# Performance work log

Hardware: AMD Instinct MI355X
Metric: run time of the kernel (lower is better)

## Reference

```python
import jax, jax.numpy as jnp
import numpy as np

B, S, D = 4, 2048, 1024
H = 16
DK = D // H  # 64
THETA = 10000.0


def setup_inputs() -> dict:
    key = jax.random.key(0)
    ks = jax.random.split(key, 5)
    scale = 1.0 / np.sqrt(D)
    return {
        "x": jax.random.normal(ks[0], (B, S, D), dtype=jnp.float32),
        "wq": jax.random.normal(ks[1], (D, D), dtype=jnp.float32) * scale,
        "wk": jax.random.normal(ks[2], (D, D), dtype=jnp.float32) * scale,
        "wv": jax.random.normal(ks[3], (D, D), dtype=jnp.float32) * scale,
        "wo": jax.random.normal(ks[4], (D, D), dtype=jnp.float32) * scale,
    }


def _rope(x, cos2, sin2):
    # x: [B, H, S, DK]; cos2/sin2: [S, DK]
    x_even = x[..., 0::2]
    x_odd = x[..., 1::2]
    x_rot = jnp.stack([-x_odd, x_even], axis=-1).reshape(x.shape)
    return x * cos2 + x_rot * sin2


def reference(x, wq, wk, wv, wo):
    b, s, d = x.shape
    # QKV projections (weights are [out, in]; y = x @ W^T)
    q = jnp.einsum("bsd,od->bso", x, wq).reshape(b, s, H, DK).swapaxes(1, 2)
    k = jnp.einsum("bsd,od->bso", x, wk).reshape(b, s, H, DK).swapaxes(1, 2)
    v = jnp.einsum("bsd,od->bso", x, wv).reshape(b, s, H, DK).swapaxes(1, 2)

    # RoPE tables for positions [0, s)
    inv_freq = 1.0 / (THETA ** (jnp.arange(0, DK, 2, dtype=jnp.float32) / DK))
    angles = jnp.arange(s, dtype=jnp.float32)[:, None] * inv_freq[None, :]  # [s, DK/2]
    cos2 = jnp.repeat(jnp.cos(angles), 2, axis=-1).astype(x.dtype)  # [s, DK]
    sin2 = jnp.repeat(jnp.sin(angles), 2, axis=-1).astype(x.dtype)
    q = _rope(q, cos2, sin2)
    k = _rope(k, cos2, sin2)

    # Naive quadratic attention with causal mask (matches source sdpa)
    scores = jnp.einsum("bhqd,bhkd->bhqk", q, k) / (DK ** 0.5)
    causal = jnp.tril(jnp.ones((s, s), dtype=jnp.float32))
    scores = jnp.where(causal == 0.0, -jnp.inf, scores)
    probs = jax.nn.softmax(scores, axis=-1)
    attn = jnp.einsum("bhqk,bhkd->bhqd", probs, v)

    attn = attn.swapaxes(1, 2).reshape(b, s, d)
    return jnp.einsum("bsd,od->bso", attn, wo)
```

## Files before the change

### kernel.cpp

```cpp
#include <hip/hip_runtime.h>


typedef _Float16 f16;
typedef _Float16 f16x4 __attribute__((ext_vector_type(4)));
typedef _Float16 f16x8 __attribute__((ext_vector_type(8)));
typedef float    f32x4 __attribute__((ext_vector_type(4)));
typedef __fp16   h16x2 __attribute__((ext_vector_type(2)));

typedef __attribute__((address_space(1))) void gvoid_t;
typedef __attribute__((address_space(3))) void lvoid_t;

#define GLD16(g, l) __builtin_amdgcn_global_load_lds( \
    (gvoid_t*)(const void*)(g), (lvoid_t*)(l), 16, 0, 0)

#define VMCNT(n) asm volatile("s_waitcnt vmcnt(" #n ")" ::: "memory")

__device__ __forceinline__ void bar() {
    __builtin_amdgcn_sched_barrier(0);
    __builtin_amdgcn_s_barrier();
    __builtin_amdgcn_sched_barrier(0);
}

constexpr int BB = 4, SS = 2048, DD = 1024, HH = 16, DKK = 64;
constexpr int MM = BB * SS;

__global__ void cvt_kernel(const float4* __restrict__ in, f16x4* __restrict__ out, int n4) {
    int stride = gridDim.x * blockDim.x;
    for (int i = blockIdx.x * blockDim.x + threadIdx.x; i < n4; i += stride) {
        float4 v = in[i];
        f16x4 o;
        o[0] = (f16)v.x; o[1] = (f16)v.y; o[2] = (f16)v.z; o[3] = (f16)v.w;
        out[i] = o;
    }
}

__global__ void cvt4_kernel(const float4* __restrict__ a, const float4* __restrict__ b,
                            const float4* __restrict__ c, const float4* __restrict__ d,
                            f16x4* __restrict__ out, int n4per) {
    const float4* srcs[4] = {a, b, c, d};
    const float4* src = srcs[blockIdx.y];
    f16x4* dst = out + (size_t)blockIdx.y * n4per;
    int stride = gridDim.x * blockDim.x;
    for (int i = blockIdx.x * blockDim.x + threadIdx.x; i < n4per; i += stride) {
        float4 v = src[i];
        f16x4 o;
        o[0] = (f16)v.x; o[1] = (f16)v.y; o[2] = (f16)v.z; o[3] = (f16)v.w;
        dst[i] = o;
    }
}

__global__ void rope_tab_kernel(float* __restrict__ ctab, float* __restrict__ stab) {
    int idx = blockIdx.x * blockDim.x + threadIdx.x;
    if (idx >= SS * DKK) return;
    int s = idx >> 6, dk = idx & 63, i = dk >> 1;
    float inv = powf(10000.0f, -(float)(2 * i) / (float)DKK);
    float ang = (float)s * inv;
    ctab[idx] = cosf(ang);
    stab[idx] = sinf(ang);
}

__device__ __forceinline__ void gemm_core(
    const f16* __restrict__ A, const f16* __restrict__ Bm,
    f16* As, f16* Bs, f32x4 (&acc)[4][4], int bm, int bn)
{
    const int tid  = threadIdx.x;
    const int lane = tid & 63, wid = tid >> 6;
    const int lrow = lane & 15, lk = lane >> 4;
    const int wm = (wid >> 1) * 64, wn = (wid & 1) * 64;

    const int r_ = tid >> 3, c_ = tid & 7;

    auto STAGE = [&](int buf, int k0) {
#pragma unroll
        for (int j = 0; j < 4; ++j) {
            int r = j * 32 + r_;
            int cs = (c_ ^ (r & 7)) * 8;
            GLD16(A  + (size_t)(bm + r) * 1024 + k0 + cs, As + buf * 8192 + (j * 256 + wid * 64) * 8);
            GLD16(Bm + (size_t)(bn + r) * 1024 + k0 + cs, Bs + buf * 8192 + (j * 256 + wid * 64) * 8);
        }
    };

    auto COMPUTE = [&](int buf) {
        const f16* Ab = As + buf * 8192;
        const f16* Bb = Bs + buf * 8192;
#pragma unroll
        for (int kk = 0; kk < 2; ++kk) {
            f16x8 af[4], bf[4];
#pragma unroll
            for (int mi = 0; mi < 4; ++mi) {
                int row = wm + mi * 16 + lrow;
                af[mi] = *(const f16x8*)&Ab[row * 64 + ((kk * 4 + lk) ^ (row & 7)) * 8];
            }
#pragma unroll
            for (int ni = 0; ni < 4; ++ni) {
                int row = wn + ni * 16 + lrow;
                bf[ni] = *(const f16x8*)&Bb[row * 64 + ((kk * 4 + lk) ^ (row & 7)) * 8];
            }
#pragma unroll
            for (int mi = 0; mi < 4; ++mi)
#pragma unroll
                for (int ni = 0; ni < 4; ++ni)
                    acc[mi][ni] = __builtin_amdgcn_mfma_f32_16x16x32_f16(
                        af[mi], bf[ni], acc[mi][ni], 0, 0, 0);
        }
    };

    STAGE(0, 0);
    int cur = 0;
#pragma unroll 1
    for (int t = 0; t < 16; ++t) {
        if (t < 15) { STAGE(cur ^ 1, (t + 1) * 64); VMCNT(8); }
        else        { VMCNT(0); }
        bar();
        COMPUTE(cur);
        bar();
        cur ^= 1;
    }
}

__global__ __launch_bounds__(256) void qkv_gemm(
    const f16* __restrict__ xb, const f16* __restrict__ wqkv,
    f16* __restrict__ Qr, f16* __restrict__ Kr, f16* __restrict__ Vt,
    const float* __restrict__ ctab, const float* __restrict__ stab)
{
    __shared__ __align__(16) f16 As[2 * 128 * 64];
    __shared__ __align__(16) f16 Bs[2 * 128 * 64];
    const int i = blockIdx.x;
    const int xcol = i >> 6;
    const int yrow = (i & 7) * 8 + ((i >> 3) & 7);
    const int bm = yrow * 128, bn = xcol * 128;
    const int z = bn >> 10;
    const int bnw = bn & 1023;

    f32x4 acc[4][4] = {};
    gemm_core(xb, wqkv, As, Bs, acc, bm, bn);

    const int tid = threadIdx.x, lane = tid & 63, wid = tid >> 6;
    const int lrow = lane & 15, lk = lane >> 4;
    const int wm = (wid >> 1) * 64, wn = (wid & 1) * 64;

    if (z == 2) {
#pragma unroll
        for (int mi = 0; mi < 4; ++mi)
#pragma unroll
            for (int ni = 0; ni < 4; ++ni)
#pragma unroll
                for (int r = 0; r < 4; ++r) {
                    int row = bm + wm + mi * 16 + lk * 4 + r;
                    int col = bnw + wn + ni * 16 + lrow;
                    int b = row >> 11, s = row & 2047, h = col >> 6, dk = col & 63;
                    Vt[((size_t)(b * HH + h) * DKK + dk) * SS + s] = (f16)acc[mi][ni][r];
                }
    } else {
        f16* Out = (z == 0) ? Qr : Kr;
        const float scale = (z == 0) ? 0.125f * 1.44269504088896f : 1.0f;
#pragma unroll
        for (int mi = 0; mi < 4; ++mi)
#pragma unroll
            for (int ni = 0; ni < 4; ++ni)
#pragma unroll
                for (int r = 0; r < 4; ++r) {
                    int row = bm + wm + mi * 16 + lk * 4 + r;
                    int col = bnw + wn + ni * 16 + lrow;
                    int b = row >> 11, s = row & 2047, h = col >> 6, dk = col & 63;
                    float v = acc[mi][ni][r];
                    float partner = __shfl_xor(v, 1);
                    float cc = ctab[s * DKK + dk], ssn = stab[s * DKK + dk];
                    float rot = (col & 1) ? partner : -partner;
                    float o = (v * cc + rot * ssn) * scale;
                    Out[((size_t)(b * HH + h) * SS + s) * DKK + dk] = (f16)o;
                }
    }
}

__global__ __launch_bounds__(256, 4) void attn_kernel(
    const f16* __restrict__ Q, const f16* __restrict__ K, const f16* __restrict__ Vt,
    f16* __restrict__ attnB)
{
    __shared__ __align__(16) f16 Ks[2][64 * 64];
    __shared__ __align__(16) f16 Vs[2][64 * 64];
    __shared__ __align__(16) f16 Ps[4][16 * 64];

    const int tid = threadIdx.x, lane = tid & 63, wid = tid >> 6;
    const int lrow = lane & 15, lk = lane >> 4;
    const int bx = blockIdx.x;
    const int qt = 15 - (bx >> 6);
    const int bh = (bx & 7) * 8 + ((bx >> 3) & 7);
    const int b = bh >> 4, h = bh & 15;

    const f16* Qb = Q  + (size_t)bh * SS * DKK;
    const f16* Kb = K  + (size_t)bh * SS * DKK;
    const f16* Vb = Vt + (size_t)bh * DKK * SS;
    f16* PsW = &Ps[wid][0];

    const int qw = qt * 128 + wid * 32;
    const int nt = 2 * qt + 2;

    f16x8 qf[2][2];
#pragma unroll
    for (int mi = 0; mi < 2; ++mi)
#pragma unroll
        for (int kk = 0; kk < 2; ++kk)
            qf[mi][kk] = *(const f16x8*)&Qb[(size_t)(qw + mi * 16 + lrow) * DKK + kk * 32 + lk * 8];

    f32x4 oacc[2][4] = {};
    float mst[2] = {-1e30f, -1e30f}, lst[2] = {0.0f, 0.0f};
    int cur = 0;

#pragma unroll
    for (int j = 0; j < 2; ++j) {
        int ci = j * 256 + tid;
        int r = ci >> 3, c = ci & 7;
        int cs = (c ^ (r & 7)) * 8;
        GLD16(Kb + (size_t)r * DKK + cs, &Ks[cur][(j * 256 + wid * 64) * 8]);
        GLD16(Vb + (size_t)r * SS  + cs, &Vs[cur][(j * 256 + wid * 64) * 8]);
    }

#pragma unroll 1
    for (int t = 0; t < nt; ++t) {
        const int kv0 = t * 64;
        if (t + 1 < nt) {
            const int kvn = kv0 + 64;
#pragma unroll
            for (int j = 0; j < 2; ++j) {
                int ci = j * 256 + tid;
                int r = ci >> 3, c = ci & 7;
                int cs = (c ^ (r & 7)) * 8;
                GLD16(Kb + (size_t)(kvn + r) * DKK + cs, &Ks[cur ^ 1][(j * 256 + wid * 64) * 8]);
                GLD16(Vb + (size_t)r * SS + kvn + cs,    &Vs[cur ^ 1][(j * 256 + wid * 64) * 8]);
            }
            VMCNT(4);
        } else {
            VMCNT(0);
        }
        bar();

        if (kv0 <= qw + 31) {
            f32x4 sacc[2][4] = {};
            __builtin_amdgcn_s_setprio(1);
#pragma unroll
            for (int kk = 0; kk < 2; ++kk)
#pragma unroll
                for (int ni = 0; ni < 4; ++ni) {
                    int row = ni * 16 + lrow;
                    f16x8 kf = *(const f16x8*)&Ks[cur][row * 64 + ((kk * 4 + lk) ^ (row & 7)) * 8];
#pragma unroll
                    for (int mi = 0; mi < 2; ++mi)
                        sacc[mi][ni] = __builtin_amdgcn_mfma_f32_16x16x32_f16(
                            kf, qf[mi][kk], sacc[mi][ni], 0, 0, 0);
                }
            __builtin_amdgcn_s_setprio(0);

#pragma unroll
            for (int mi = 0; mi < 2; ++mi) {
                const int q = qw + mi * 16 + lrow;
                if (kv0 + 63 > q) {
#pragma unroll
                    for (int ni = 0; ni < 4; ++ni)
#pragma unroll
                        for (int r = 0; r < 4; ++r)
                            if (kv0 + ni * 16 + lk * 4 + r > q) sacc[mi][ni][r] = -1e30f;
                }
                float m0 = -1e30f;
#pragma unroll
                for (int ni = 0; ni < 4; ++ni) {
                    float a = fmaxf(sacc[mi][ni][0], sacc[mi][ni][1]);
                    float bx2 = fmaxf(sacc[mi][ni][2], sacc[mi][ni][3]);
                    m0 = fmaxf(m0, fmaxf(a, bx2));
                }
                m0 = fmaxf(m0, __shfl_xor(m0, 16));
                m0 = fmaxf(m0, __shfl_xor(m0, 32));
                if (!__all(m0 - mst[mi] <= 11.5f)) {
                    const float mnew  = fmaxf(mst[mi], m0);
                    const float alpha = exp2f(mst[mi] - mnew);
                    mst[mi] = mnew;
                    lst[mi] *= alpha;
#pragma unroll
                    for (int no = 0; no < 4; ++no)
#pragma unroll
                        for (int r = 0; r < 4; ++r)
                            oacc[mi][no][r] *= alpha;
                }
                const float mref = mst[mi];
                float rsum = 0.0f;
#pragma unroll
                for (int ni = 0; ni < 4; ++ni) {
                    float p0 = exp2f(sacc[mi][ni][0] - mref);
                    float p1 = exp2f(sacc[mi][ni][1] - mref);
                    float p2 = exp2f(sacc[mi][ni][2] - mref);
                    float p3 = exp2f(sacc[mi][ni][3] - mref);
                    rsum += (p0 + p1) + (p2 + p3);
                    h16x2 w0 = __builtin_amdgcn_cvt_pkrtz(p0, p1);
                    h16x2 w1 = __builtin_amdgcn_cvt_pkrtz(p2, p3);
                    f16x4 w;
                    w[0] = (f16)w0[0]; w[1] = (f16)w0[1];
                    w[2] = (f16)w1[0]; w[3] = (f16)w1[1];
                    const int c = ni * 2 + (lk >> 1);
                    *(f16x4*)&PsW[lrow * 64 + ((c ^ (lrow & 7)) * 8) + (lk & 1) * 4] = w;
                }
                rsum += __shfl_xor(rsum, 16);
                rsum += __shfl_xor(rsum, 32);
                lst[mi] += rsum;

                f16x8 pa[2];
#pragma unroll
                for (int kk = 0; kk < 2; ++kk)
                    pa[kk] = *(const f16x8*)&PsW[lrow * 64 + ((kk * 4 + lk) ^ (lrow & 7)) * 8];
                __builtin_amdgcn_s_setprio(1);
#pragma unroll
                for (int kk = 0; kk < 2; ++kk)
#pragma unroll
                    for (int no = 0; no < 4; ++no) {
                        int row = no * 16 + lrow;
                        f16x8 vf = *(const f16x8*)&Vs[cur][row * 64 + ((kk * 4 + lk) ^ (row & 7)) * 8];
                        oacc[mi][no] = __builtin_amdgcn_mfma_f32_16x16x32_f16(
                            vf, pa[kk], oacc[mi][no], 0, 0, 0);
                    }
                __builtin_amdgcn_s_setprio(0);
            }
        }

        bar();
        cur ^= 1;
    }

#pragma unroll
    for (int mi = 0; mi < 2; ++mi) {
        const float rl = 1.0f / lst[mi];
        const int q = qw + mi * 16 + lrow;
#pragma unroll
        for (int no = 0; no < 4; ++no) {
            f16x4 w;
#pragma unroll
            for (int r = 0; r < 4; ++r) w[r] = (f16)(oacc[mi][no][r] * rl);
            *(f16x4*)&attnB[((size_t)(b * SS) + q) * DD + h * DKK + no * 16 + lk * 4] = w;
        }
    }
}

__global__ __launch_bounds__(256) void out_gemm(
    const f16* __restrict__ attnB, const f16* __restrict__ wob, float* __restrict__ out)
{
    __shared__ __align__(16) f16 As[2 * 128 * 64];
    __shared__ __align__(16) f16 Bs[2 * 128 * 64];
    const int i = blockIdx.x;
    const int xcol = i >> 6;
    const int yrow = (i & 7) * 8 + ((i >> 3) & 7);
    const int bm = yrow * 128, bn = xcol * 128;
    f32x4 acc[4][4] = {};
    gemm_core(attnB, wob, As, Bs, acc, bm, bn);
    const int tid = threadIdx.x, lane = tid & 63, wid = tid >> 6;
    const int lrow = lane & 15, lk = lane >> 4;
    const int wm = (wid >> 1) * 64, wn = (wid & 1) * 64;
#pragma unroll
    for (int mi = 0; mi < 4; ++mi)
#pragma unroll
        for (int ni = 0; ni < 4; ++ni)
#pragma unroll
            for (int r = 0; r < 4; ++r) {
                int row = bm + wm + mi * 16 + lk * 4 + r;
                int col = bn + wn + ni * 16 + lrow;
                out[(size_t)row * 1024 + col] = acc[mi][ni][r];
            }
}

extern "C" void kernel_launch(void* const* d_in, const int* in_sizes, int n_in,
                              void* d_out, int out_size, void* d_ws, size_t ws_size,
                              hipStream_t stream) {
    const float* x  = (const float*)d_in[0];
    const float* wq = (const float*)d_in[1];
    const float* wk = (const float*)d_in[2];
    const float* wv = (const float*)d_in[3];
    const float* wo = (const float*)d_in[4];
    float* out = (float*)d_out;

    constexpr size_t NXB = (size_t)MM * DD;
    constexpr size_t NW  = (size_t)DD * DD;
    f16* xb  = (f16*)d_ws;
    f16* wqkv = xb + NXB;
    f16* wob  = wqkv + 3 * NW;
    f16* Qr  = wob + NW;
    f16* Kr  = Qr  + NXB;
    f16* Vt  = Kr  + NXB;
    float* ctab = (float*)(Vt + NXB);
    float* stab = ctab + SS * DKK;
    f16* attnB = xb;

    cvt_kernel<<<2048, 256, 0, stream>>>((const float4*)x, (f16x4*)xb, (int)(NXB / 4));
    cvt4_kernel<<<dim3(512, 4), 256, 0, stream>>>((const float4*)wq, (const float4*)wk,
                                                  (const float4*)wv, (const float4*)wo,
                                                  (f16x4*)wqkv, (int)(NW / 4));
    rope_tab_kernel<<<(SS * DKK + 255) / 256, 256, 0, stream>>>(ctab, stab);

    qkv_gemm<<<1536, 256, 0, stream>>>(xb, wqkv, Qr, Kr, Vt, ctab, stab);
    attn_kernel<<<1024, 256, 0, stream>>>(Qr, Kr, Vt, attnB);
    out_gemm<<<512, 256, 0, stream>>>(attnB, wob, out);
}
```

Measured before the change: 207.3 us.

## Shrink attention query tile to 64 rows, one 16-row slab per wave

The attention kernel now gives each block 64 query rows instead of 128, with each wave handling 16 rows instead of 32, and launches twice as many blocks. The causal-skip branch and the setprio hints are removed, since every wave's tile now intersects every loaded KV tile. This doubles parallelism and cuts the wasted causal work per block. In exchange, K/V tiles are reused by half as many query rows, so K/V global traffic doubles and each LDS K/V read feeds fewer MFMAs.

Result: faster. 179.0 us (-13.7%).

```diff
diff --git a/kernel.cpp b/kernel.cpp
--- a/kernel.cpp
+++ b/kernel.cpp
@@ -184,7 +184,7 @@
     const int tid = threadIdx.x, lane = tid & 63, wid = tid >> 6;
     const int lrow = lane & 15, lk = lane >> 4;
     const int bx = blockIdx.x;
-    const int qt = 15 - (bx >> 6);
+    const int qt = 31 - (bx >> 6);
     const int bh = (bx & 7) * 8 + ((bx >> 3) & 7);
     const int b = bh >> 4, h = bh & 15;
 
@@ -193,18 +193,17 @@
     const f16* Vb = Vt + (size_t)bh * DKK * SS;
     f16* PsW = &Ps[wid][0];
 
-    const int qw = qt * 128 + wid * 32;
-    const int nt = 2 * qt + 2;
-
-    f16x8 qf[2][2];
-#pragma unroll
-    for (int mi = 0; mi < 2; ++mi)
-#pragma unroll
-        for (int kk = 0; kk < 2; ++kk)
-            qf[mi][kk] = *(const f16x8*)&Qb[(size_t)(qw + mi * 16 + lrow) * DKK + kk * 32 + lk * 8];
-
-    f32x4 oacc[2][4] = {};
-    float mst[2] = {-1e30f, -1e30f}, lst[2] = {0.0f, 0.0f};
+    const int qw = qt * 64 + wid * 16;
+    const int nt = qt + 1;
+    const int q  = qw + lrow;
+
+    f16x8 qf[2];
+#pragma unroll
+    for (int kk = 0; kk < 2; ++kk)
+        qf[kk] = *(const f16x8*)&Qb[(size_t)q * DKK + kk * 32 + lk * 8];
+
+    f32x4 oacc[4] = {};
+    float mst = -1e30f, lst = 0.0f;
     int cur = 0;
 
 #pragma unroll
@@ -235,104 +234,90 @@
         }
         bar();
 
-        if (kv0 <= qw + 31) {
-            f32x4 sacc[2][4] = {};
-            __builtin_amdgcn_s_setprio(1);
-#pragma unroll
-            for (int kk = 0; kk < 2; ++kk)
-#pragma unroll
-                for (int ni = 0; ni < 4; ++ni) {
-                    int row = ni * 16 + lrow;
-                    f16x8 kf = *(const f16x8*)&Ks[cur][row * 64 + ((kk * 4 + lk) ^ (row & 7)) * 8];
-#pragma unroll
-                    for (int mi = 0; mi < 2; ++mi)
-                        sacc[mi][ni] = __builtin_amdgcn_mfma_f32_16x16x32_f16(
-                            kf, qf[mi][kk], sacc[mi][ni], 0, 0, 0);
-                }
-            __builtin_amdgcn_s_setprio(0);
-
-#pragma unroll
-            for (int mi = 0; mi < 2; ++mi) {
-                const int q = qw + mi * 16 + lrow;
-                if (kv0 + 63 > q) {
-#pragma unroll
-                    for (int ni = 0; ni < 4; ++ni)
-#pragma unroll
-                        for (int r = 0; r < 4; ++r)
-                            if (kv0 + ni * 16 + lk * 4 + r > q) sacc[mi][ni][r] = -1e30f;
-                }
-                float m0 = -1e30f;
-#pragma unroll
-                for (int ni = 0; ni < 4; ++ni) {
-                    float a = fmaxf(sacc[mi][ni][0], sacc[mi][ni][1]);
-                    float bx2 = fmaxf(sacc[mi][ni][2], sacc[mi][ni][3]);
-                    m0 = fmaxf(m0, fmaxf(a, bx2));
-                }
-                m0 = fmaxf(m0, __shfl_xor(m0, 16));
-                m0 = fmaxf(m0, __shfl_xor(m0, 32));
-                if (!__all(m0 - mst[mi] <= 11.5f)) {
-                    const float mnew  = fmaxf(mst[mi], m0);
-                    const float alpha = exp2f(mst[mi] - mnew);
-                    mst[mi] = mnew;
-                    lst[mi] *= alpha;
-#pragma unroll
-                    for (int no = 0; no < 4; ++no)
-#pragma unroll
-                        for (int r = 0; r < 4; ++r)
-                            oacc[mi][no][r] *= alpha;
-                }
-                const float mref = mst[mi];
-                float rsum = 0.0f;
-#pragma unroll
-                for (int ni = 0; ni < 4; ++ni) {
-                    float p0 = exp2f(sacc[mi][ni][0] - mref);
-                    float p1 = exp2f(sacc[mi][ni][1] - mref);
-                    float p2 = exp2f(sacc[mi][ni][2] - mref);
-                    float p3 = exp2f(sacc[mi][ni][3] - mref);
-                    rsum += (p0 + p1) + (p2 + p3);
-                    h16x2 w0 = __builtin_amdgcn_cvt_pkrtz(p0, p1);
-                    h16x2 w1 = __builtin_amdgcn_cvt_pkrtz(p2, p3);
-                    f16x4 w;
-                    w[0] = (f16)w0[0]; w[1] = (f16)w0[1];
-                    w[2] = (f16)w1[0]; w[3] = (f16)w1[1];
-                    const int c = ni * 2 + (lk >> 1);
-                    *(f16x4*)&PsW[lrow * 64 + ((c ^ (lrow & 7)) * 8) + (lk & 1) * 4] = w;
-                }
-                rsum += __shfl_xor(rsum, 16);
-                rsum += __shfl_xor(rsum, 32);
-                lst[mi] += rsum;
-
-                f16x8 pa[2];
-#pragma unroll
-                for (int kk = 0; kk < 2; ++kk)
-                    pa[kk] = *(const f16x8*)&PsW[lrow * 64 + ((kk * 4 + lk) ^ (lrow & 7)) * 8];
-                __builtin_amdgcn_s_setprio(1);
-#pragma unroll
-                for (int kk = 0; kk < 2; ++kk)
-#pragma unroll
-                    for (int no = 0; no < 4; ++no) {
-                        int row = no * 16 + lrow;
-                        f16x8 vf = *(const f16x8*)&Vs[cur][row * 64 + ((kk * 4 + lk) ^ (row & 7)) * 8];
-                        oacc[mi][no] = __builtin_amdgcn_mfma_f32_16x16x32_f16(
-                            vf, pa[kk], oacc[mi][no], 0, 0, 0);
-                    }
-                __builtin_amdgcn_s_setprio(0);
-            }
-        }
+        f32x4 sacc[4] = {};
+#pragma unroll
+        for (int kk = 0; kk < 2; ++kk)
+#pragma unroll
+            for (int ni = 0; ni < 4; ++ni) {
+                int row = ni * 16 + lrow;
+                f16x8 kf = *(const f16x8*)&Ks[cur][row * 64 + ((kk * 4 + lk) ^ (row & 7)) * 8];
+                sacc[ni] = __builtin_amdgcn_mfma_f32_16x16x32_f16(
+                    kf, qf[kk], sacc[ni], 0, 0, 0);
+            }
+
+        if (kv0 + 63 > q) {
+#pragma unroll
+            for (int ni = 0; ni < 4; ++ni)
+#pragma unroll
+                for (int r = 0; r < 4; ++r)
+                    if (kv0 + ni * 16 + lk * 4 + r > q) sacc[ni][r] = -1e30f;
+        }
+        float m0 = -1e30f;
+#pragma unroll
+        for (int ni = 0; ni < 4; ++ni) {
+            float a  = fmaxf(sacc[ni][0], sacc[ni][1]);
+            float b2 = fmaxf(sacc[ni][2], sacc[ni][3]);
+            m0 = fmaxf(m0, fmaxf(a, b2));
+        }
+        m0 = fmaxf(m0, __shfl_xor(m0, 16));
+        m0 = fmaxf(m0, __shfl_xor(m0, 32));
+        if (!__all(m0 - mst <= 11.5f)) {
+            const float mnew  = fmaxf(mst, m0);
+            const float alpha = exp2f(mst - mnew);
+            mst = mnew;
+            lst *= alpha;
+#pragma unroll
+            for (int no = 0; no < 4; ++no)
+#pragma unroll
+                for (int r = 0; r < 4; ++r)
+                    oacc[no][r] *= alpha;
+        }
+        const float mref = mst;
+        float rsum = 0.0f;
+#pragma unroll
+        for (int ni = 0; ni < 4; ++ni) {
+            float p0 = exp2f(sacc[ni][0] - mref);
+            float p1 = exp2f(sacc[ni][1] - mref);
+            float p2 = exp2f(sacc[ni][2] - mref);
+            float p3 = exp2f(sacc[ni][3] - mref);
+            rsum += (p0 + p1) + (p2 + p3);
+            h16x2 w0 = __builtin_amdgcn_cvt_pkrtz(p0, p1);
+            h16x2 w1 = __builtin_amdgcn_cvt_pkrtz(p2, p3);
+            f16x4 w;
+            w[0] = (f16)w0[0]; w[1] = (f16)w0[1];
+            w[2] = (f16)w1[0]; w[3] = (f16)w1[1];
+            const int c = ni * 2 + (lk >> 1);
+            *(f16x4*)&PsW[lrow * 64 + ((c ^ (lrow & 7)) * 8) + (lk & 1) * 4] = w;
+        }
+        rsum += __shfl_xor(rsum, 16);
+        rsum += __shfl_xor(rsum, 32);
+        lst += rsum;
+
+        f16x8 pa[2];
+#pragma unroll
+        for (int kk = 0; kk < 2; ++kk)
+            pa[kk] = *(const f16x8*)&PsW[lrow * 64 + ((kk * 4 + lk) ^ (lrow & 7)) * 8];
+#pragma unroll
+        for (int kk = 0; kk < 2; ++kk)
+#pragma unroll
+            for (int no = 0; no < 4; ++no) {
+                int row = no * 16 + lrow;
+                f16x8 vf = *(const f16x8*)&Vs[cur][row * 64 + ((kk * 4 + lk) ^ (row & 7)) * 8];
+                oacc[no] = __builtin_amdgcn_mfma_f32_16x16x32_f16(
+                    vf, pa[kk], oacc[no], 0, 0, 0);
+            }
 
         bar();
         cur ^= 1;
     }
 
-#pragma unroll
-    for (int mi = 0; mi < 2; ++mi) {
-        const float rl = 1.0f / lst[mi];
-        const int q = qw + mi * 16 + lrow;
+    {
+        const float rl = 1.0f / lst;
 #pragma unroll
         for (int no = 0; no < 4; ++no) {
             f16x4 w;
 #pragma unroll
-            for (int r = 0; r < 4; ++r) w[r] = (f16)(oacc[mi][no][r] * rl);
+            for (int r = 0; r < 4; ++r) w[r] = (f16)(oacc[no][r] * rl);
             *(f16x4*)&attnB[((size_t)(b * SS) + q) * DD + h * DKK + no * 16 + lk * 4] = w;
         }
     }
@@ -393,6 +378,6 @@
     rope_tab_kernel<<<(SS * DKK + 255) / 256, 256, 0, stream>>>(ctab, stab);
 
     qkv_gemm<<<1536, 256, 0, stream>>>(xb, wqkv, Qr, Kr, Vt, ctab, stab);
-    attn_kernel<<<1024, 256, 0, stream>>>(Qr, Kr, Vt, attnB);
+    attn_kernel<<<2048, 256, 0, stream>>>(Qr, Kr, Vt, attnB);
     out_gemm<<<512, 256, 0, stream>>>(attnB, wob, out);
 }
```
